# Optimization experiments

Measured on AMD Instinct MI355X. Metric: run time of the kernel, lower is better.

## Reference

```python
import jax, jax.numpy as jnp
import numpy as np

BEV_H, BEV_W, BEV_Z = 128, 128, 16
N_VOX = BEV_H * BEV_W * BEV_Z  # 262144
C = 128
N_UNMASKED = N_VOX // 4       # 65536 seed voxels (proposal > 0)
LN_EPS = 1e-5
NEG_SLOPE = 0.01


def setup_inputs() -> dict:
    key = jax.random.key(0)
    ks = jax.random.split(key, 8)
    x3d = jax.random.normal(ks[0], (1, C, N_VOX), dtype=jnp.float32)
    # disjoint unmasked/masked index sets from a permutation (proposal mask)
    perm = jax.random.permutation(ks[1], N_VOX)
    unmasked_idx = jnp.sort(perm[:N_UNMASKED]).astype(jnp.int32)
    masked_idx = jnp.sort(perm[N_UNMASKED:]).astype(jnp.int32)
    s = 0.05
    return {
        "x3d": x3d,
        "w1": jax.random.normal(ks[2], (C, C // 2), jnp.float32) * s,
        "b1": jnp.zeros((C // 2,), jnp.float32),
        "ln_g": jnp.ones((C // 2,), jnp.float32),
        "ln_b": jnp.zeros((C // 2,), jnp.float32),
        "w2": jax.random.normal(ks[3], (C // 2, C), jnp.float32) * s,
        "b2": jnp.zeros((C,), jnp.float32),
        "sdb_w": jax.random.normal(ks[4], (C, C // 2), jnp.float32) * s,
        "sdb_b": jnp.zeros((C // 2,), jnp.float32),
        "ssc_w": jax.random.normal(ks[5], (C // 2, 20), jnp.float32) * s,
        "ssc_b": jnp.zeros((20,), jnp.float32),
        "aux_w": jax.random.normal(ks[6], (C, 20), jnp.float32) * s,
        "aux_b": jnp.zeros((20,), jnp.float32),
        "unmasked_idx": unmasked_idx,
        "masked_idx": masked_idx,
    }


def _leaky(x):
    return jnp.where(x > 0, x, NEG_SLOPE * x)


def _layernorm(x, g, b):
    mu = jnp.mean(x, axis=-1, keepdims=True)
    var = jnp.mean(jnp.square(x - mu), axis=-1, keepdims=True)
    return (x - mu) * jax.lax.rsqrt(var + LN_EPS) * g + b


def reference(x3d, w1, b1, ln_g, ln_b, w2, b2, sdb_w, sdb_b, ssc_w, ssc_b,
              aux_w, aux_b, unmasked_idx, masked_idx):
    feats = x3d[0].T  # [N_vox, C]
    # gather seed (unmasked) voxel features; SGB treated as identity stand-in
    seed_feats = feats[unmasked_idx]            # [Nu, C]
    # gather masked voxel features and infill with mlp_prior:
    # Linear -> LayerNorm -> LeakyReLU -> Linear
    m = feats[masked_idx]                       # [Nm, C]
    h = _leaky(_layernorm(m @ w1 + b1, ln_g, ln_b))
    prior = h @ w2 + b2                         # [Nm, C]
    # scatter both into the dense voxel grid
    vox = jnp.zeros((N_VOX, C), x3d.dtype)
    vox = vox.at[unmasked_idx].set(seed_feats).at[masked_idx].set(prior)
    # SDB dense decode stand-in: pointwise conv C -> C/2 + LeakyReLU
    d = _leaky(vox @ sdb_w + sdb_b)             # [N_vox, C/2]
    # ssc head: per-voxel logits -> [1, 20, H, W, Z]
    ssc = d @ ssc_w + ssc_b                     # [N_vox, 20]
    ssc_logit = ssc.reshape(BEV_H, BEV_W, BEV_Z, 20).transpose(3, 0, 1, 2)[None]
    # aux sparse head on seed features
    sem_logit = seed_feats @ aux_w + aux_b      # [Nu, 20]
    return ssc_logit, sem_logit
```

## Files before the change

kernel.cpp:

```cpp
#include <hip/hip_runtime.h>
#include <hip/hip_bf16.h>


#define NVOX 262144
#define NU   65536
#define NM   196608
#define CIN  128
#define CHALF 64
#define NCLS 20
#define TR   64
#define NBLK (NVOX / TR)

#define SXS 136
#define SHS 72
#define SOS 21

#define W1F  0
#define W2F  8192
#define SDBF 16384
#define SSCF 24576
#define AUXF 26624
#define WS_WT 30720

typedef unsigned short u16;
typedef short    bf16x8 __attribute__((ext_vector_type(8)));
typedef float    f32x4  __attribute__((ext_vector_type(4)));

__device__ __forceinline__ u16 f2b(float f) {
    __hip_bfloat16 h = __float2bfloat16(f);
    return *(u16*)&h;
}

__global__ void prep_weights(const float* __restrict__ w1,  const float* __restrict__ w2,
                             const float* __restrict__ sdbw,const float* __restrict__ sscw,
                             const float* __restrict__ auxw,
                             const int* __restrict__ uidx,  const int* __restrict__ midx,
                             u16* __restrict__ ws) {
    int i = blockIdx.x * blockDim.x + threadIdx.x;
    const int stride = gridDim.x * blockDim.x;
    int* __restrict__ rank = (int*)(ws + WS_WT);
    for (int t = i; t < NU; t += stride) rank[uidx[t]] = t;
    for (int t = i; t < NM; t += stride) rank[midx[t]] = -1;
    for (; i < WS_WT; i += stride) {
        float v;
        if (i < W2F) {
            int t = i, j = t & 7, lane = (t >> 3) & 63, kc = (t >> 9) & 3, nt = t >> 11;
            int k = kc*32 + (lane >> 4)*8 + j, n = nt*16 + (lane & 15);
            v = w1[k*CHALF + n];
        } else if (i < SDBF) {
            int t = i - W2F, j = t & 7, lane = (t >> 3) & 63, kc = (t >> 9) & 1, nt = t >> 10;
            int k = kc*32 + (lane >> 4)*8 + j, n = nt*16 + (lane & 15);
            v = w2[k*CIN + n];
        } else if (i < SSCF) {
            int t = i - SDBF, j = t & 7, lane = (t >> 3) & 63, kc = (t >> 9) & 3, nt = t >> 11;
            int k = kc*32 + (lane >> 4)*8 + j, n = nt*16 + (lane & 15);
            v = sdbw[k*CHALF + n];
        } else if (i < AUXF) {
            int t = i - SSCF, j = t & 7, lane = (t >> 3) & 63, kc = (t >> 9) & 1, nt = t >> 10;
            int k = kc*32 + (lane >> 4)*8 + j, n = nt*16 + (lane & 15);
            v = (n < NCLS) ? sscw[k*NCLS + n] : 0.f;
        } else {
            int t = i - AUXF, j = t & 7, lane = (t >> 3) & 63, kc = (t >> 9) & 3, nt = t >> 11;
            int k = kc*32 + (lane >> 4)*8 + j, n = nt*16 + (lane & 15);
            v = (n < NCLS) ? auxw[k*NCLS + n] : 0.f;
        }
        ws[i] = f2b(v);
    }
}

__global__ __launch_bounds__(256, 4)
void sgn_mfma(const float* __restrict__ x3d,
              const float* __restrict__ b1,   const float* __restrict__ lng,
              const float* __restrict__ lnb,  const float* __restrict__ bb2,
              const float* __restrict__ sdbb, const float* __restrict__ sscb,
              const float* __restrict__ auxb,
              const int* __restrict__ rank,   const u16* __restrict__ wt,
              float* __restrict__ out)
{
    __shared__ __align__(16) u16 sX[TR * SXS];
    __shared__ __align__(16) u16 sH[TR * SHS];
    __shared__ __align__(16) float sOut[TR * SOS];
    __shared__ int sRank[TR];

    const int tid = threadIdx.x;
    const int p0  = (int)blockIdx.x * TR;

    const int g  = tid >> 4;
    const int v0 = (tid & 15) * 4;
    f32x4 va[4], vb[4];
    #pragma unroll
    for (int i = 0; i < 4; ++i) {
        const int c0 = i*32 + g*2;
        va[i] = *(const f32x4*)&x3d[(size_t)c0      * NVOX + p0 + v0];
        vb[i] = *(const f32x4*)&x3d[(size_t)(c0+1)  * NVOX + p0 + v0];
    }

    if (tid < TR) sRank[tid] = rank[p0 + tid];

    #pragma unroll
    for (int i = 0; i < 4; ++i) {
        const int c0 = i*32 + g*2;
        #pragma unroll
        for (int j = 0; j < 4; ++j) {
            unsigned pk = (unsigned)f2b(va[i][j]) | ((unsigned)f2b(vb[i][j]) << 16);
            *(unsigned*)&sX[(v0 + j)*SXS + c0] = pk;
        }
    }
    __syncthreads();

    const int m0   = (tid >> 6) * 16;
    const int lane = tid & 63;
    const int q    = lane >> 4;
    const int n15  = lane & 15;
    const int kq   = q * 8;


    {
        f32x4 acc[4];
        #pragma unroll
        for (int nt = 0; nt < 4; ++nt) {
            const float b = b1[nt*16 + n15];
            acc[nt] = (f32x4){b, b, b, b};
        }
        #pragma unroll
        for (int kc = 0; kc < 4; ++kc) {
            const bf16x8 a = *(const bf16x8*)&sX[(m0 + n15) * SXS + kc*32 + kq];
            #pragma unroll
            for (int nt = 0; nt < 4; ++nt) {
                const bf16x8 b = *(const bf16x8*)&wt[W1F + ((nt*4 + kc)*64 + lane)*8];
                acc[nt] = __builtin_amdgcn_mfma_f32_16x16x32_bf16(a, b, acc[nt], 0, 0, 0);
            }
        }
        float gv[4], ev[4];
        #pragma unroll
        for (int nt = 0; nt < 4; ++nt) { gv[nt] = lng[nt*16 + n15]; ev[nt] = lnb[nt*16 + n15]; }
        #pragma unroll
        for (int reg = 0; reg < 4; ++reg) {
            float s1 = acc[0][reg] + acc[1][reg] + acc[2][reg] + acc[3][reg];
            float s2 = acc[0][reg]*acc[0][reg] + acc[1][reg]*acc[1][reg]
                     + acc[2][reg]*acc[2][reg] + acc[3][reg]*acc[3][reg];
            #pragma unroll
            for (int m = 1; m <= 8; m <<= 1) {
                s1 += __shfl_xor(s1, m, 64);
                s2 += __shfl_xor(s2, m, 64);
            }
            const float mu  = s1 * (1.f/64.f);
            const float var = s2 * (1.f/64.f) - mu*mu;
            const float rs  = rsqrtf(var + 1e-5f);
            #pragma unroll
            for (int nt = 0; nt < 4; ++nt) {
                float h = (acc[nt][reg] - mu) * rs * gv[nt] + ev[nt];
                h = h > 0.f ? h : 0.01f*h;
                sH[(m0 + q*4 + reg) * SHS + nt*16 + n15] = f2b(h);
            }
        }
    }

    {
        f32x4 acc2[8];
        #pragma unroll
        for (int nt = 0; nt < 8; ++nt) {
            const float b = bb2[nt*16 + n15];
            acc2[nt] = (f32x4){b, b, b, b};
        }
        #pragma unroll
        for (int kc = 0; kc < 2; ++kc) {
            const bf16x8 a = *(const bf16x8*)&sH[(m0 + n15) * SHS + kc*32 + kq];
            #pragma unroll
            for (int nt = 0; nt < 8; ++nt) {
                const bf16x8 b = *(const bf16x8*)&wt[W2F + ((nt*2 + kc)*64 + lane)*8];
                acc2[nt] = __builtin_amdgcn_mfma_f32_16x16x32_bf16(a, b, acc2[nt], 0, 0, 0);
            }
        }
        #pragma unroll
        for (int reg = 0; reg < 4; ++reg) {
            const int row = m0 + q*4 + reg;
            if (sRank[row] < 0) {
                #pragma unroll
                for (int nt = 0; nt < 8; ++nt)
                    sX[row * SXS + nt*16 + n15] = f2b(acc2[nt][reg]);
            }
        }
    }

    {
        f32x4 accd[4];
        #pragma unroll
        for (int nt = 0; nt < 4; ++nt) {
            const float b = sdbb[nt*16 + n15];
            accd[nt] = (f32x4){b, b, b, b};
        }
        #pragma unroll
        for (int kc = 0; kc < 4; ++kc) {
            const bf16x8 a = *(const bf16x8*)&sX[(m0 + n15) * SXS + kc*32 + kq];
            #pragma unroll
            for (int nt = 0; nt < 4; ++nt) {
                const bf16x8 b = *(const bf16x8*)&wt[SDBF + ((nt*4 + kc)*64 + lane)*8];
                accd[nt] = __builtin_amdgcn_mfma_f32_16x16x32_bf16(a, b, accd[nt], 0, 0, 0);
            }
        }
        #pragma unroll
        for (int reg = 0; reg < 4; ++reg)
            #pragma unroll
            for (int nt = 0; nt < 4; ++nt) {
                float vv = accd[nt][reg];
                vv = vv > 0.f ? vv : 0.01f*vv;
                sH[(m0 + q*4 + reg) * SHS + nt*16 + n15] = f2b(vv);
            }
    }

    {
        f32x4 accs[2];
        #pragma unroll
        for (int nt = 0; nt < 2; ++nt) {
            const int col = nt*16 + n15;
            const float b = (col < NCLS) ? sscb[col] : 0.f;
            accs[nt] = (f32x4){b, b, b, b};
        }
        #pragma unroll
        for (int kc = 0; kc < 2; ++kc) {
            const bf16x8 a = *(const bf16x8*)&sH[(m0 + n15) * SHS + kc*32 + kq];
            #pragma unroll
            for (int nt = 0; nt < 2; ++nt) {
                const bf16x8 b = *(const bf16x8*)&wt[SSCF + ((nt*2 + kc)*64 + lane)*8];
                accs[nt] = __builtin_amdgcn_mfma_f32_16x16x32_bf16(a, b, accs[nt], 0, 0, 0);
            }
        }
        #pragma unroll
        for (int reg = 0; reg < 4; ++reg) {
            const int row = m0 + q*4 + reg;
            sOut[row*SOS + n15] = accs[0][reg];
            if (n15 < 4) sOut[row*SOS + 16 + n15] = accs[1][reg];
        }
    }

    f32x4 acca[2];
    {
        #pragma unroll
        for (int nt = 0; nt < 2; ++nt) {
            const int col = nt*16 + n15;
            const float b = (col < NCLS) ? auxb[col] : 0.f;
            acca[nt] = (f32x4){b, b, b, b};
        }
        #pragma unroll
        for (int kc = 0; kc < 4; ++kc) {
            const bf16x8 a = *(const bf16x8*)&sX[(m0 + n15) * SXS + kc*32 + kq];
            #pragma unroll
            for (int nt = 0; nt < 2; ++nt) {
                const bf16x8 b = *(const bf16x8*)&wt[AUXF + ((nt*4 + kc)*64 + lane)*8];
                acca[nt] = __builtin_amdgcn_mfma_f32_16x16x32_bf16(a, b, acca[nt], 0, 0, 0);
            }
        }
    }
    __syncthreads();

    #pragma unroll
    for (int jj = 0; jj < 5; ++jj) {
        const int i = tid + jj*256;
        out[(size_t)(i >> 6) * NVOX + p0 + (i & 63)] = sOut[(i & 63) * SOS + (i >> 6)];
    }

    {
        const size_t base = (size_t)NCLS * NVOX;
        #pragma unroll
        for (int reg = 0; reg < 4; ++reg) {
            const int row = m0 + q*4 + reg;
            const int rk  = sRank[row];
            if (rk >= 0) {
                out[base + (size_t)rk * NCLS + n15] = acca[0][reg];
                if (n15 < 4)
                    out[base + (size_t)rk * NCLS + 16 + n15] = acca[1][reg];
            }
        }
    }
}

extern "C" void kernel_launch(void* const* d_in, const int* in_sizes, int n_in,
                              void* d_out, int out_size, void* d_ws, size_t ws_size,
                              hipStream_t stream) {
    const float* x3d  = (const float*)d_in[0];
    const float* w1   = (const float*)d_in[1];
    const float* b1   = (const float*)d_in[2];
    const float* lng  = (const float*)d_in[3];
    const float* lnb  = (const float*)d_in[4];
    const float* w2   = (const float*)d_in[5];
    const float* bb2  = (const float*)d_in[6];
    const float* sdbw = (const float*)d_in[7];
    const float* sdbb = (const float*)d_in[8];
    const float* sscw = (const float*)d_in[9];
    const float* sscb = (const float*)d_in[10];
    const float* auxw = (const float*)d_in[11];
    const float* auxb = (const float*)d_in[12];
    const int*   uidx = (const int*)d_in[13];
    const int*   midx = (const int*)d_in[14];
    float* out = (float*)d_out;
    u16*   wt  = (u16*)d_ws;
    const int* rank = (const int*)((const char*)d_ws + WS_WT*2);

    hipLaunchKernelGGL(prep_weights, dim3(128), dim3(256), 0, stream,
                       w1, w2, sdbw, sscw, auxw, uidx, midx, wt);
    hipLaunchKernelGGL(sgn_mfma, dim3(NBLK), dim3(256), 0, stream,
                       x3d, b1, lng, lnb, bb2, sdbb, sscb, auxb,
                       rank, wt, out);
}
```

Measured before the change: 250.1 us.

## Process four tiles per block with register prefetch of next tile

Each block now loops over four 64-voxel tiles. The next tile's x3d loads and rank go into registers before the current tile's MFMA chain starts, so global load latency overlaps compute. Output stores become nontemporal, and launch bounds drop to 2 blocks per CU to make room for the prefetch registers. The cost is fewer blocks, lower occupancy and an extra barrier per tile.

```diff
diff --git a/kernel.cpp b/kernel.cpp
--- a/kernel.cpp
+++ b/kernel.cpp
@@ -9,7 +9,8 @@
 #define CHALF 64
 #define NCLS 20
 #define TR   64
-#define NBLK (NVOX / TR)
+#define TILES 4
+#define NBLK (NVOX / (TR * TILES))
 
 #define SXS 136
 #define SHS 72
@@ -68,7 +69,7 @@
     }
 }
 
-__global__ __launch_bounds__(256, 4)
+__global__ __launch_bounds__(256, 2)
 void sgn_mfma(const float* __restrict__ x3d,
               const float* __restrict__ b1,   const float* __restrict__ lng,
               const float* __restrict__ lnb,  const float* __restrict__ bb2,
@@ -82,20 +83,22 @@
     __shared__ __align__(16) float sOut[TR * SOS];
     __shared__ int sRank[TR];
 
-    const int tid = threadIdx.x;
-    const int p0  = (int)blockIdx.x * TR;
+    const int tid  = threadIdx.x;
+    const int base = (int)blockIdx.x * (TR * TILES);
 
     const int g  = tid >> 4;
     const int v0 = (tid & 15) * 4;
+
     f32x4 va[4], vb[4];
+    int rkreg = -1;
+
     #pragma unroll
     for (int i = 0; i < 4; ++i) {
         const int c0 = i*32 + g*2;
-        va[i] = *(const f32x4*)&x3d[(size_t)c0      * NVOX + p0 + v0];
-        vb[i] = *(const f32x4*)&x3d[(size_t)(c0+1)  * NVOX + p0 + v0];
+        va[i] = *(const f32x4*)&x3d[(size_t)c0      * NVOX + base + v0];
+        vb[i] = *(const f32x4*)&x3d[(size_t)(c0+1)  * NVOX + base + v0];
     }
-
-    if (tid < TR) sRank[tid] = rank[p0 + tid];
+    if (tid < TR) rkreg = rank[base + tid];
 
     #pragma unroll
     for (int i = 0; i < 4; ++i) {
@@ -106,6 +109,7 @@
             *(unsigned*)&sX[(v0 + j)*SXS + c0] = pk;
         }
     }
+    if (tid < TR) sRank[tid] = rkreg;
     __syncthreads();
 
     const int m0   = (tid >> 6) * 16;
@@ -114,164 +118,199 @@
     const int n15  = lane & 15;
     const int kq   = q * 8;
 
-
-    {
-        f32x4 acc[4];
+    #pragma unroll 1
+    for (int t = 0; t < TILES; ++t) {
+        const int p0 = base + t * TR;
+
+        if (t + 1 < TILES) {
+            #pragma unroll
+            for (int i = 0; i < 4; ++i) {
+                const int c0 = i*32 + g*2;
+                va[i] = *(const f32x4*)&x3d[(size_t)c0      * NVOX + p0 + TR + v0];
+                vb[i] = *(const f32x4*)&x3d[(size_t)(c0+1)  * NVOX + p0 + TR + v0];
+            }
+            if (tid < TR) rkreg = rank[p0 + TR + tid];
+        }
+
+        {
+            f32x4 acc[4];
+            #pragma unroll
+            for (int nt = 0; nt < 4; ++nt) {
+                const float b = b1[nt*16 + n15];
+                acc[nt] = (f32x4){b, b, b, b};
+            }
+            #pragma unroll
+            for (int kc = 0; kc < 4; ++kc) {
+                const bf16x8 a = *(const bf16x8*)&sX[(m0 + n15) * SXS + kc*32 + kq];
+                #pragma unroll
+                for (int nt = 0; nt < 4; ++nt) {
+                    const bf16x8 b = *(const bf16x8*)&wt[W1F + ((nt*4 + kc)*64 + lane)*8];
+                    acc[nt] = __builtin_amdgcn_mfma_f32_16x16x32_bf16(a, b, acc[nt], 0, 0, 0);
+                }
+            }
+            float gv[4], ev[4];
+            #pragma unroll
+            for (int nt = 0; nt < 4; ++nt) { gv[nt] = lng[nt*16 + n15]; ev[nt] = lnb[nt*16 + n15]; }
+            #pragma unroll
+            for (int reg = 0; reg < 4; ++reg) {
+                float s1 = acc[0][reg] + acc[1][reg] + acc[2][reg] + acc[3][reg];
+                float s2 = acc[0][reg]*acc[0][reg] + acc[1][reg]*acc[1][reg]
+                         + acc[2][reg]*acc[2][reg] + acc[3][reg]*acc[3][reg];
+                #pragma unroll
+                for (int m = 1; m <= 8; m <<= 1) {
+                    s1 += __shfl_xor(s1, m, 64);
+                    s2 += __shfl_xor(s2, m, 64);
+                }
+                const float mu  = s1 * (1.f/64.f);
+                const float var = s2 * (1.f/64.f) - mu*mu;
+                const float rs  = rsqrtf(var + 1e-5f);
+                #pragma unroll
+                for (int nt = 0; nt < 4; ++nt) {
+                    float h = (acc[nt][reg] - mu) * rs * gv[nt] + ev[nt];
+                    h = h > 0.f ? h : 0.01f*h;
+                    sH[(m0 + q*4 + reg) * SHS + nt*16 + n15] = f2b(h);
+                }
+            }
+        }
+
+        {
+            f32x4 acc2[8];
+            #pragma unroll
+            for (int nt = 0; nt < 8; ++nt) {
+                const float b = bb2[nt*16 + n15];
+                acc2[nt] = (f32x4){b, b, b, b};
+            }
+            #pragma unroll
+            for (int kc = 0; kc < 2; ++kc) {
+                const bf16x8 a = *(const bf16x8*)&sH[(m0 + n15) * SHS + kc*32 + kq];
+                #pragma unroll
+                for (int nt = 0; nt < 8; ++nt) {
+                    const bf16x8 b = *(const bf16x8*)&wt[W2F + ((nt*2 + kc)*64 + lane)*8];
+                    acc2[nt] = __builtin_amdgcn_mfma_f32_16x16x32_bf16(a, b, acc2[nt], 0, 0, 0);
+                }
+            }
+            #pragma unroll
+            for (int reg = 0; reg < 4; ++reg) {
+                const int row = m0 + q*4 + reg;
+                if (sRank[row] < 0) {
+                    #pragma unroll
+                    for (int nt = 0; nt < 8; ++nt)
+                        sX[row * SXS + nt*16 + n15] = f2b(acc2[nt][reg]);
+                }
+            }
+        }
+
+        {
+            f32x4 accd[4];
+            #pragma unroll
+            for (int nt = 0; nt < 4; ++nt) {
+                const float b = sdbb[nt*16 + n15];
+                accd[nt] = (f32x4){b, b, b, b};
+            }
+            #pragma unroll
+            for (int kc = 0; kc < 4; ++kc) {
+                const bf16x8 a = *(const bf16x8*)&sX[(m0 + n15) * SXS + kc*32 + kq];
+                #pragma unroll
+                for (int nt = 0; nt < 4; ++nt) {
+                    const bf16x8 b = *(const bf16x8*)&wt[SDBF + ((nt*4 + kc)*64 + lane)*8];
+                    accd[nt] = __builtin_amdgcn_mfma_f32_16x16x32_bf16(a, b, accd[nt], 0, 0, 0);
+                }
+            }
+            #pragma unroll
+            for (int reg = 0; reg < 4; ++reg)
+                #pragma unroll
+                for (int nt = 0; nt < 4; ++nt) {
+                    float vv = accd[nt][reg];
+                    vv = vv > 0.f ? vv : 0.01f*vv;
+                    sH[(m0 + q*4 + reg) * SHS + nt*16 + n15] = f2b(vv);
+                }
+        }
+
+        {
+            f32x4 accs[2];
+            #pragma unroll
+            for (int nt = 0; nt < 2; ++nt) {
+                const int col = nt*16 + n15;
+                const float b = (col < NCLS) ? sscb[col] : 0.f;
+                accs[nt] = (f32x4){b, b, b, b};
+            }
+            #pragma unroll
+            for (int kc = 0; kc < 2; ++kc) {
+                const bf16x8 a = *(const bf16x8*)&sH[(m0 + n15) * SHS + kc*32 + kq];
+                #pragma unroll
+                for (int nt = 0; nt < 2; ++nt) {
+                    const bf16x8 b = *(const bf16x8*)&wt[SSCF + ((nt*2 + kc)*64 + lane)*8];
+                    accs[nt] = __builtin_amdgcn_mfma_f32_16x16x32_bf16(a, b, accs[nt], 0, 0, 0);
+                }
+            }
+            #pragma unroll
+            for (int reg = 0; reg < 4; ++reg) {
+                const int row = m0 + q*4 + reg;
+                sOut[row*SOS + n15] = accs[0][reg];
+                if (n15 < 4) sOut[row*SOS + 16 + n15] = accs[1][reg];
+            }
+        }
+
+        f32x4 acca[2];
+        {
+            #pragma unroll
+            for (int nt = 0; nt < 2; ++nt) {
+                const int col = nt*16 + n15;
+                const float b = (col < NCLS) ? auxb[col] : 0.f;
+                acca[nt] = (f32x4){b, b, b, b};
+            }
+            #pragma unroll
+            for (int kc = 0; kc < 4; ++kc) {
+                const bf16x8 a = *(const bf16x8*)&sX[(m0 + n15) * SXS + kc*32 + kq];
+                #pragma unroll
+                for (int nt = 0; nt < 2; ++nt) {
+                    const bf16x8 b = *(const bf16x8*)&wt[AUXF + ((nt*4 + kc)*64 + lane)*8];
+                    acca[nt] = __builtin_amdgcn_mfma_f32_16x16x32_bf16(a, b, acca[nt], 0, 0, 0);
+                }
+            }
+        }
+
+        int rk4[4];
         #pragma unroll
-        for (int nt = 0; nt < 4; ++nt) {
-            const float b = b1[nt*16 + n15];
-            acc[nt] = (f32x4){b, b, b, b};
-        }
+        for (int reg = 0; reg < 4; ++reg) rk4[reg] = sRank[m0 + q*4 + reg];
+
+        __syncthreads();
+
         #pragma unroll
-        for (int kc = 0; kc < 4; ++kc) {
-            const bf16x8 a = *(const bf16x8*)&sX[(m0 + n15) * SXS + kc*32 + kq];
-            #pragma unroll
-            for (int nt = 0; nt < 4; ++nt) {
-                const bf16x8 b = *(const bf16x8*)&wt[W1F + ((nt*4 + kc)*64 + lane)*8];
-                acc[nt] = __builtin_amdgcn_mfma_f32_16x16x32_bf16(a, b, acc[nt], 0, 0, 0);
-            }
-        }
-        float gv[4], ev[4];
-        #pragma unroll
-        for (int nt = 0; nt < 4; ++nt) { gv[nt] = lng[nt*16 + n15]; ev[nt] = lnb[nt*16 + n15]; }
-        #pragma unroll
-        for (int reg = 0; reg < 4; ++reg) {
-            float s1 = acc[0][reg] + acc[1][reg] + acc[2][reg] + acc[3][reg];
-            float s2 = acc[0][reg]*acc[0][reg] + acc[1][reg]*acc[1][reg]
-                     + acc[2][reg]*acc[2][reg] + acc[3][reg]*acc[3][reg];
-            #pragma unroll
-            for (int m = 1; m <= 8; m <<= 1) {
-                s1 += __shfl_xor(s1, m, 64);
-                s2 += __shfl_xor(s2, m, 64);
-            }
-            const float mu  = s1 * (1.f/64.f);
-            const float var = s2 * (1.f/64.f) - mu*mu;
-            const float rs  = rsqrtf(var + 1e-5f);
-            #pragma unroll
-            for (int nt = 0; nt < 4; ++nt) {
-                float h = (acc[nt][reg] - mu) * rs * gv[nt] + ev[nt];
-                h = h > 0.f ? h : 0.01f*h;
-                sH[(m0 + q*4 + reg) * SHS + nt*16 + n15] = f2b(h);
-            }
-        }
-    }
-
-    {
-        f32x4 acc2[8];
-        #pragma unroll
-        for (int nt = 0; nt < 8; ++nt) {
-            const float b = bb2[nt*16 + n15];
-            acc2[nt] = (f32x4){b, b, b, b};
-        }
-        #pragma unroll
-        for (int kc = 0; kc < 2; ++kc) {
-            const bf16x8 a = *(const bf16x8*)&sH[(m0 + n15) * SHS + kc*32 + kq];
-            #pragma unroll
-            for (int nt = 0; nt < 8; ++nt) {
-                const bf16x8 b = *(const bf16x8*)&wt[W2F + ((nt*2 + kc)*64 + lane)*8];
-                acc2[nt] = __builtin_amdgcn_mfma_f32_16x16x32_bf16(a, b, acc2[nt], 0, 0, 0);
-            }
-        }
-        #pragma unroll
-        for (int reg = 0; reg < 4; ++reg) {
-            const int row = m0 + q*4 + reg;
-            if (sRank[row] < 0) {
-                #pragma unroll
-                for (int nt = 0; nt < 8; ++nt)
-                    sX[row * SXS + nt*16 + n15] = f2b(acc2[nt][reg]);
-            }
-        }
-    }
-
-    {
-        f32x4 accd[4];
-        #pragma unroll
-        for (int nt = 0; nt < 4; ++nt) {
-            const float b = sdbb[nt*16 + n15];
-            accd[nt] = (f32x4){b, b, b, b};
-        }
-        #pragma unroll
-        for (int kc = 0; kc < 4; ++kc) {
-            const bf16x8 a = *(const bf16x8*)&sX[(m0 + n15) * SXS + kc*32 + kq];
-            #pragma unroll
-            for (int nt = 0; nt < 4; ++nt) {
-                const bf16x8 b = *(const bf16x8*)&wt[SDBF + ((nt*4 + kc)*64 + lane)*8];
-                accd[nt] = __builtin_amdgcn_mfma_f32_16x16x32_bf16(a, b, accd[nt], 0, 0, 0);
-            }
-        }
-        #pragma unroll
-        for (int reg = 0; reg < 4; ++reg)
-            #pragma unroll
-            for (int nt = 0; nt < 4; ++nt) {
-                float vv = accd[nt][reg];
-                vv = vv > 0.f ? vv : 0.01f*vv;
-                sH[(m0 + q*4 + reg) * SHS + nt*16 + n15] = f2b(vv);
-            }
-    }
-
-    {
-        f32x4 accs[2];
-        #pragma unroll
-        for (int nt = 0; nt < 2; ++nt) {
-            const int col = nt*16 + n15;
-            const float b = (col < NCLS) ? sscb[col] : 0.f;
-            accs[nt] = (f32x4){b, b, b, b};
-        }
-        #pragma unroll
-        for (int kc = 0; kc < 2; ++kc) {
-            const bf16x8 a = *(const bf16x8*)&sH[(m0 + n15) * SHS + kc*32 + kq];
-            #pragma unroll
-            for (int nt = 0; nt < 2; ++nt) {
-                const bf16x8 b = *(const bf16x8*)&wt[SSCF + ((nt*2 + kc)*64 + lane)*8];
-                accs[nt] = __builtin_amdgcn_mfma_f32_16x16x32_bf16(a, b, accs[nt], 0, 0, 0);
-            }
-        }
-        #pragma unroll
-        for (int reg = 0; reg < 4; ++reg) {
-            const int row = m0 + q*4 + reg;
-            sOut[row*SOS + n15] = accs[0][reg];
-            if (n15 < 4) sOut[row*SOS + 16 + n15] = accs[1][reg];
-        }
-    }
-
-    f32x4 acca[2];
-    {
-        #pragma unroll
-        for (int nt = 0; nt < 2; ++nt) {
-            const int col = nt*16 + n15;
-            const float b = (col < NCLS) ? auxb[col] : 0.f;
-            acca[nt] = (f32x4){b, b, b, b};
-        }
-        #pragma unroll
-        for (int kc = 0; kc < 4; ++kc) {
-            const bf16x8 a = *(const bf16x8*)&sX[(m0 + n15) * SXS + kc*32 + kq];
-            #pragma unroll
-            for (int nt = 0; nt < 2; ++nt) {
-                const bf16x8 b = *(const bf16x8*)&wt[AUXF + ((nt*4 + kc)*64 + lane)*8];
-                acca[nt] = __builtin_amdgcn_mfma_f32_16x16x32_bf16(a, b, acca[nt], 0, 0, 0);
-            }
-        }
-    }
-    __syncthreads();
-
-    #pragma unroll
-    for (int jj = 0; jj < 5; ++jj) {
-        const int i = tid + jj*256;
-        out[(size_t)(i >> 6) * NVOX + p0 + (i & 63)] = sOut[(i & 63) * SOS + (i >> 6)];
-    }
-
-    {
-        const size_t base = (size_t)NCLS * NVOX;
-        #pragma unroll
-        for (int reg = 0; reg < 4; ++reg) {
-            const int row = m0 + q*4 + reg;
-            const int rk  = sRank[row];
-            if (rk >= 0) {
-                out[base + (size_t)rk * NCLS + n15] = acca[0][reg];
-                if (n15 < 4)
-                    out[base + (size_t)rk * NCLS + 16 + n15] = acca[1][reg];
-            }
-        }
+        for (int jj = 0; jj < 5; ++jj) {
+            const int i = tid + jj*256;
+            __builtin_nontemporal_store(sOut[(i & 63) * SOS + (i >> 6)],
+                &out[(size_t)(i >> 6) * NVOX + p0 + (i & 63)]);
+        }
+
+        {
+            const size_t abase = (size_t)NCLS * NVOX;
+            #pragma unroll
+            for (int reg = 0; reg < 4; ++reg) {
+                const int rk = rk4[reg];
+                if (rk >= 0) {
+                    __builtin_nontemporal_store(acca[0][reg],
+                        &out[abase + (size_t)rk * NCLS + n15]);
+                    if (n15 < 4)
+                        __builtin_nontemporal_store(acca[1][reg],
+                            &out[abase + (size_t)rk * NCLS + 16 + n15]);
+                }
+            }
+        }
+
+        if (t + 1 < TILES) {
+            #pragma unroll
+            for (int i = 0; i < 4; ++i) {
+                const int c0 = i*32 + g*2;
+                #pragma unroll
+                for (int j = 0; j < 4; ++j) {
+                    unsigned pk = (unsigned)f2b(va[i][j]) | ((unsigned)f2b(vb[i][j]) << 16);
+                    *(unsigned*)&sX[(v0 + j)*SXS + c0] = pk;
+                }
+            }
+            if (tid < TR) sRank[tid] = rkreg;
+        }
+        __syncthreads();
     }
 }
 
```

Result: slower. 397.7 us (+59.0%).

## Double rows per block so each wave reuses weight fragments across two M-tiles

Applied to the files above, without the earlier changes.

Block tile grows from 64 to 128 voxels, and each wave now computes two 16-row MFMA tiles that share every weight fragment load from global memory. This halves weight fetches per voxel and gives each wave more independent MFMAs to interleave. The load stage now converts each chunk straight into LDS instead of holding all loads in registers first, and the aux stores move before the final barrier. The cost is more registers and LDS per block, with launch bounds lowered to 2 blocks per SM, so occupancy and latency hiding may drop.

```diff
diff --git a/kernel.cpp b/kernel.cpp
--- a/kernel.cpp
+++ b/kernel.cpp
@@ -8,7 +8,7 @@
 #define CIN  128
 #define CHALF 64
 #define NCLS 20
-#define TR   64
+#define TR   128
 #define NBLK (NVOX / TR)
 
 #define SXS 136
@@ -68,7 +68,7 @@
     }
 }
 
-__global__ __launch_bounds__(256, 4)
+__global__ __launch_bounds__(256, 2)
 void sgn_mfma(const float* __restrict__ x3d,
               const float* __restrict__ b1,   const float* __restrict__ lng,
               const float* __restrict__ lnb,  const float* __restrict__ bb2,
@@ -85,193 +85,206 @@
     const int tid = threadIdx.x;
     const int p0  = (int)blockIdx.x * TR;
 
-    const int g  = tid >> 4;
-    const int v0 = (tid & 15) * 4;
-    f32x4 va[4], vb[4];
+    const int g  = tid >> 5;
+    const int v0 = (tid & 31) * 4;
     #pragma unroll
-    for (int i = 0; i < 4; ++i) {
-        const int c0 = i*32 + g*2;
-        va[i] = *(const f32x4*)&x3d[(size_t)c0      * NVOX + p0 + v0];
-        vb[i] = *(const f32x4*)&x3d[(size_t)(c0+1)  * NVOX + p0 + v0];
-    }
-
+    for (int i = 0; i < 8; ++i) {
+        const int c0 = g*2 + 16*i;
+        f32x4 va = *(const f32x4*)&x3d[(size_t)c0     * NVOX + p0 + v0];
+        f32x4 vb = *(const f32x4*)&x3d[(size_t)(c0+1) * NVOX + p0 + v0];
+        #pragma unroll
+        for (int j = 0; j < 4; ++j) {
+            unsigned pk = (unsigned)f2b(va[j]) | ((unsigned)f2b(vb[j]) << 16);
+            *(unsigned*)&sX[(v0 + j)*SXS + c0] = pk;
+        }
+    }
     if (tid < TR) sRank[tid] = rank[p0 + tid];
-
-    #pragma unroll
-    for (int i = 0; i < 4; ++i) {
-        const int c0 = i*32 + g*2;
-        #pragma unroll
-        for (int j = 0; j < 4; ++j) {
-            unsigned pk = (unsigned)f2b(va[i][j]) | ((unsigned)f2b(vb[i][j]) << 16);
-            *(unsigned*)&sX[(v0 + j)*SXS + c0] = pk;
-        }
-    }
     __syncthreads();
 
-    const int m0   = (tid >> 6) * 16;
+    const int W0   = (tid >> 6) * 32;
     const int lane = tid & 63;
     const int q    = lane >> 4;
     const int n15  = lane & 15;
     const int kq   = q * 8;
 
-
-    {
-        f32x4 acc[4];
+    {
+        f32x4 acc[2][4];
         #pragma unroll
         for (int nt = 0; nt < 4; ++nt) {
             const float b = b1[nt*16 + n15];
-            acc[nt] = (f32x4){b, b, b, b};
+            acc[0][nt] = (f32x4){b, b, b, b};
+            acc[1][nt] = (f32x4){b, b, b, b};
         }
         #pragma unroll
         for (int kc = 0; kc < 4; ++kc) {
-            const bf16x8 a = *(const bf16x8*)&sX[(m0 + n15) * SXS + kc*32 + kq];
+            const bf16x8 a0 = *(const bf16x8*)&sX[(W0      + n15) * SXS + kc*32 + kq];
+            const bf16x8 a1 = *(const bf16x8*)&sX[(W0 + 16 + n15) * SXS + kc*32 + kq];
             #pragma unroll
             for (int nt = 0; nt < 4; ++nt) {
                 const bf16x8 b = *(const bf16x8*)&wt[W1F + ((nt*4 + kc)*64 + lane)*8];
-                acc[nt] = __builtin_amdgcn_mfma_f32_16x16x32_bf16(a, b, acc[nt], 0, 0, 0);
+                acc[0][nt] = __builtin_amdgcn_mfma_f32_16x16x32_bf16(a0, b, acc[0][nt], 0, 0, 0);
+                acc[1][nt] = __builtin_amdgcn_mfma_f32_16x16x32_bf16(a1, b, acc[1][nt], 0, 0, 0);
             }
         }
         float gv[4], ev[4];
         #pragma unroll
         for (int nt = 0; nt < 4; ++nt) { gv[nt] = lng[nt*16 + n15]; ev[nt] = lnb[nt*16 + n15]; }
         #pragma unroll
-        for (int reg = 0; reg < 4; ++reg) {
-            float s1 = acc[0][reg] + acc[1][reg] + acc[2][reg] + acc[3][reg];
-            float s2 = acc[0][reg]*acc[0][reg] + acc[1][reg]*acc[1][reg]
-                     + acc[2][reg]*acc[2][reg] + acc[3][reg]*acc[3][reg];
-            #pragma unroll
-            for (int m = 1; m <= 8; m <<= 1) {
-                s1 += __shfl_xor(s1, m, 64);
-                s2 += __shfl_xor(s2, m, 64);
-            }
-            const float mu  = s1 * (1.f/64.f);
-            const float var = s2 * (1.f/64.f) - mu*mu;
-            const float rs  = rsqrtf(var + 1e-5f);
-            #pragma unroll
-            for (int nt = 0; nt < 4; ++nt) {
-                float h = (acc[nt][reg] - mu) * rs * gv[nt] + ev[nt];
-                h = h > 0.f ? h : 0.01f*h;
-                sH[(m0 + q*4 + reg) * SHS + nt*16 + n15] = f2b(h);
-            }
-        }
-    }
-
-    {
-        f32x4 acc2[8];
+        for (int mm = 0; mm < 2; ++mm)
+            #pragma unroll
+            for (int reg = 0; reg < 4; ++reg) {
+                float s1 = acc[mm][0][reg] + acc[mm][1][reg] + acc[mm][2][reg] + acc[mm][3][reg];
+                float s2 = acc[mm][0][reg]*acc[mm][0][reg] + acc[mm][1][reg]*acc[mm][1][reg]
+                         + acc[mm][2][reg]*acc[mm][2][reg] + acc[mm][3][reg]*acc[mm][3][reg];
+                #pragma unroll
+                for (int m = 1; m <= 8; m <<= 1) {
+                    s1 += __shfl_xor(s1, m, 64);
+                    s2 += __shfl_xor(s2, m, 64);
+                }
+                const float mu  = s1 * (1.f/64.f);
+                const float var = s2 * (1.f/64.f) - mu*mu;
+                const float rs  = rsqrtf(var + 1e-5f);
+                #pragma unroll
+                for (int nt = 0; nt < 4; ++nt) {
+                    float h = (acc[mm][nt][reg] - mu) * rs * gv[nt] + ev[nt];
+                    h = h > 0.f ? h : 0.01f*h;
+                    sH[(W0 + mm*16 + q*4 + reg) * SHS + nt*16 + n15] = f2b(h);
+                }
+            }
+    }
+
+    {
+        f32x4 acc2[2][8];
         #pragma unroll
         for (int nt = 0; nt < 8; ++nt) {
             const float b = bb2[nt*16 + n15];
-            acc2[nt] = (f32x4){b, b, b, b};
+            acc2[0][nt] = (f32x4){b, b, b, b};
+            acc2[1][nt] = (f32x4){b, b, b, b};
         }
         #pragma unroll
         for (int kc = 0; kc < 2; ++kc) {
-            const bf16x8 a = *(const bf16x8*)&sH[(m0 + n15) * SHS + kc*32 + kq];
+            const bf16x8 a0 = *(const bf16x8*)&sH[(W0      + n15) * SHS + kc*32 + kq];
+            const bf16x8 a1 = *(const bf16x8*)&sH[(W0 + 16 + n15) * SHS + kc*32 + kq];
             #pragma unroll
             for (int nt = 0; nt < 8; ++nt) {
                 const bf16x8 b = *(const bf16x8*)&wt[W2F + ((nt*2 + kc)*64 + lane)*8];
-                acc2[nt] = __builtin_amdgcn_mfma_f32_16x16x32_bf16(a, b, acc2[nt], 0, 0, 0);
-            }
-        }
-        #pragma unroll
-        for (int reg = 0; reg < 4; ++reg) {
-            const int row = m0 + q*4 + reg;
-            if (sRank[row] < 0) {
-                #pragma unroll
-                for (int nt = 0; nt < 8; ++nt)
-                    sX[row * SXS + nt*16 + n15] = f2b(acc2[nt][reg]);
-            }
-        }
-    }
-
-    {
-        f32x4 accd[4];
+                acc2[0][nt] = __builtin_amdgcn_mfma_f32_16x16x32_bf16(a0, b, acc2[0][nt], 0, 0, 0);
+                acc2[1][nt] = __builtin_amdgcn_mfma_f32_16x16x32_bf16(a1, b, acc2[1][nt], 0, 0, 0);
+            }
+        }
+        #pragma unroll
+        for (int mm = 0; mm < 2; ++mm)
+            #pragma unroll
+            for (int reg = 0; reg < 4; ++reg) {
+                const int row = W0 + mm*16 + q*4 + reg;
+                if (sRank[row] < 0) {
+                    #pragma unroll
+                    for (int nt = 0; nt < 8; ++nt)
+                        sX[row * SXS + nt*16 + n15] = f2b(acc2[mm][nt][reg]);
+                }
+            }
+    }
+
+    {
+        f32x4 accd[2][4];
         #pragma unroll
         for (int nt = 0; nt < 4; ++nt) {
             const float b = sdbb[nt*16 + n15];
-            accd[nt] = (f32x4){b, b, b, b};
+            accd[0][nt] = (f32x4){b, b, b, b};
+            accd[1][nt] = (f32x4){b, b, b, b};
         }
         #pragma unroll
         for (int kc = 0; kc < 4; ++kc) {
-            const bf16x8 a = *(const bf16x8*)&sX[(m0 + n15) * SXS + kc*32 + kq];
+            const bf16x8 a0 = *(const bf16x8*)&sX[(W0      + n15) * SXS + kc*32 + kq];
+            const bf16x8 a1 = *(const bf16x8*)&sX[(W0 + 16 + n15) * SXS + kc*32 + kq];
             #pragma unroll
             for (int nt = 0; nt < 4; ++nt) {
                 const bf16x8 b = *(const bf16x8*)&wt[SDBF + ((nt*4 + kc)*64 + lane)*8];
-                accd[nt] = __builtin_amdgcn_mfma_f32_16x16x32_bf16(a, b, accd[nt], 0, 0, 0);
-            }
-        }
-        #pragma unroll
-        for (int reg = 0; reg < 4; ++reg)
-            #pragma unroll
-            for (int nt = 0; nt < 4; ++nt) {
-                float vv = accd[nt][reg];
-                vv = vv > 0.f ? vv : 0.01f*vv;
-                sH[(m0 + q*4 + reg) * SHS + nt*16 + n15] = f2b(vv);
-            }
-    }
-
-    {
-        f32x4 accs[2];
+                accd[0][nt] = __builtin_amdgcn_mfma_f32_16x16x32_bf16(a0, b, accd[0][nt], 0, 0, 0);
+                accd[1][nt] = __builtin_amdgcn_mfma_f32_16x16x32_bf16(a1, b, accd[1][nt], 0, 0, 0);
+            }
+        }
+        #pragma unroll
+        for (int mm = 0; mm < 2; ++mm)
+            #pragma unroll
+            for (int reg = 0; reg < 4; ++reg)
+                #pragma unroll
+                for (int nt = 0; nt < 4; ++nt) {
+                    float vv = accd[mm][nt][reg];
+                    vv = vv > 0.f ? vv : 0.01f*vv;
+                    sH[(W0 + mm*16 + q*4 + reg) * SHS + nt*16 + n15] = f2b(vv);
+                }
+    }
+
+    {
+        f32x4 accs[2][2];
         #pragma unroll
         for (int nt = 0; nt < 2; ++nt) {
             const int col = nt*16 + n15;
             const float b = (col < NCLS) ? sscb[col] : 0.f;
-            accs[nt] = (f32x4){b, b, b, b};
+            accs[0][nt] = (f32x4){b, b, b, b};
+            accs[1][nt] = (f32x4){b, b, b, b};
         }
         #pragma unroll
         for (int kc = 0; kc < 2; ++kc) {
-            const bf16x8 a = *(const bf16x8*)&sH[(m0 + n15) * SHS + kc*32 + kq];
+            const bf16x8 a0 = *(const bf16x8*)&sH[(W0      + n15) * SHS + kc*32 + kq];
+            const bf16x8 a1 = *(const bf16x8*)&sH[(W0 + 16 + n15) * SHS + kc*32 + kq];
             #pragma unroll
             for (int nt = 0; nt < 2; ++nt) {
                 const bf16x8 b = *(const bf16x8*)&wt[SSCF + ((nt*2 + kc)*64 + lane)*8];
-                accs[nt] = __builtin_amdgcn_mfma_f32_16x16x32_bf16(a, b, accs[nt], 0, 0, 0);
-            }
-        }
-        #pragma unroll
-        for (int reg = 0; reg < 4; ++reg) {
-            const int row = m0 + q*4 + reg;
-            sOut[row*SOS + n15] = accs[0][reg];
-            if (n15 < 4) sOut[row*SOS + 16 + n15] = accs[1][reg];
-        }
-    }
-
-    f32x4 acca[2];
-    {
+                accs[0][nt] = __builtin_amdgcn_mfma_f32_16x16x32_bf16(a0, b, accs[0][nt], 0, 0, 0);
+                accs[1][nt] = __builtin_amdgcn_mfma_f32_16x16x32_bf16(a1, b, accs[1][nt], 0, 0, 0);
+            }
+        }
+        #pragma unroll
+        for (int mm = 0; mm < 2; ++mm)
+            #pragma unroll
+            for (int reg = 0; reg < 4; ++reg) {
+                const int row = W0 + mm*16 + q*4 + reg;
+                sOut[row*SOS + n15] = accs[mm][0][reg];
+                if (n15 < 4) sOut[row*SOS + 16 + n15] = accs[mm][1][reg];
+            }
+    }
+
+    {
+        f32x4 acca[2][2];
         #pragma unroll
         for (int nt = 0; nt < 2; ++nt) {
             const int col = nt*16 + n15;
             const float b = (col < NCLS) ? auxb[col] : 0.f;
-            acca[nt] = (f32x4){b, b, b, b};
+            acca[0][nt] = (f32x4){b, b, b, b};
+            acca[1][nt] = (f32x4){b, b, b, b};
         }
         #pragma unroll
         for (int kc = 0; kc < 4; ++kc) {
-            const bf16x8 a = *(const bf16x8*)&sX[(m0 + n15) * SXS + kc*32 + kq];
+            const bf16x8 a0 = *(const bf16x8*)&sX[(W0      + n15) * SXS + kc*32 + kq];
+            const bf16x8 a1 = *(const bf16x8*)&sX[(W0 + 16 + n15) * SXS + kc*32 + kq];
             #pragma unroll
             for (int nt = 0; nt < 2; ++nt) {
                 const bf16x8 b = *(const bf16x8*)&wt[AUXF + ((nt*4 + kc)*64 + lane)*8];
-                acca[nt] = __builtin_amdgcn_mfma_f32_16x16x32_bf16(a, b, acca[nt], 0, 0, 0);
-            }
-        }
+                acca[0][nt] = __builtin_amdgcn_mfma_f32_16x16x32_bf16(a0, b, acca[0][nt], 0, 0, 0);
+                acca[1][nt] = __builtin_amdgcn_mfma_f32_16x16x32_bf16(a1, b, acca[1][nt], 0, 0, 0);
+            }
+        }
+        const size_t abase = (size_t)NCLS * NVOX;
+        #pragma unroll
+        for (int mm = 0; mm < 2; ++mm)
+            #pragma unroll
+            for (int reg = 0; reg < 4; ++reg) {
+                const int rk = sRank[W0 + mm*16 + q*4 + reg];
+                if (rk >= 0) {
+                    out[abase + (size_t)rk * NCLS + n15] = acca[mm][0][reg];
+                    if (n15 < 4)
+                        out[abase + (size_t)rk * NCLS + 16 + n15] = acca[mm][1][reg];
+                }
+            }
     }
     __syncthreads();
 
     #pragma unroll
-    for (int jj = 0; jj < 5; ++jj) {
+    for (int jj = 0; jj < 10; ++jj) {
         const int i = tid + jj*256;
-        out[(size_t)(i >> 6) * NVOX + p0 + (i & 63)] = sOut[(i & 63) * SOS + (i >> 6)];
-    }
-
-    {
-        const size_t base = (size_t)NCLS * NVOX;
-        #pragma unroll
-        for (int reg = 0; reg < 4; ++reg) {
-            const int row = m0 + q*4 + reg;
-            const int rk  = sRank[row];
-            if (rk >= 0) {
-                out[base + (size_t)rk * NCLS + n15] = acca[0][reg];
-                if (n15 < 4)
-                    out[base + (size_t)rk * NCLS + 16 + n15] = acca[1][reg];
-            }
-        }
+        out[(size_t)(i >> 7) * NVOX + p0 + (i & 127)] = sOut[(i & 127) * SOS + (i >> 7)];
     }
 }
 
```

Result: slower. 261.9 us (+4.7%).

## Make blocks persistent over eight tiles with async global-to-LDS prefetch

Applied to the files above, without the earlier changes.

Each block now handles eight 64-voxel tiles in a loop instead of one. The next tile's x3d slice is prefetched directly into an LDS staging buffer with global_load_lds, and the rank values are double-buffered, so load latency overlaps with the MFMA chain of the current tile. The aux head is fused into the first GEMM's K loop, reusing the same A fragments. LDS grows by 32 KB and launch bounds drop to 2 blocks per SM, which trades occupancy for explicit overlap and leaves fewer blocks to fill the GPU.

```diff
diff --git a/kernel.cpp b/kernel.cpp
--- a/kernel.cpp
+++ b/kernel.cpp
@@ -9,7 +9,8 @@
 #define CHALF 64
 #define NCLS 20
 #define TR   64
-#define NBLK (NVOX / TR)
+#define TILES 8
+#define NBLK (NVOX / (TR * TILES))
 
 #define SXS 136
 #define SHS 72
@@ -68,7 +69,7 @@
     }
 }
 
-__global__ __launch_bounds__(256, 4)
+__global__ __launch_bounds__(256, 2)
 void sgn_mfma(const float* __restrict__ x3d,
               const float* __restrict__ b1,   const float* __restrict__ lng,
               const float* __restrict__ lnb,  const float* __restrict__ bb2,
@@ -77,201 +78,220 @@
               const int* __restrict__ rank,   const u16* __restrict__ wt,
               float* __restrict__ out)
 {
+    __shared__ __align__(16) float sStage[CIN * TR];
     __shared__ __align__(16) u16 sX[TR * SXS];
     __shared__ __align__(16) u16 sH[TR * SHS];
     __shared__ __align__(16) float sOut[TR * SOS];
-    __shared__ int sRank[TR];
-
-    const int tid = threadIdx.x;
-    const int p0  = (int)blockIdx.x * TR;
-
-    const int g  = tid >> 4;
-    const int v0 = (tid & 15) * 4;
-    f32x4 va[4], vb[4];
-    #pragma unroll
-    for (int i = 0; i < 4; ++i) {
-        const int c0 = i*32 + g*2;
-        va[i] = *(const f32x4*)&x3d[(size_t)c0      * NVOX + p0 + v0];
-        vb[i] = *(const f32x4*)&x3d[(size_t)(c0+1)  * NVOX + p0 + v0];
-    }
-
-    if (tid < TR) sRank[tid] = rank[p0 + tid];
-
-    #pragma unroll
-    for (int i = 0; i < 4; ++i) {
-        const int c0 = i*32 + g*2;
+    __shared__ int sRank[2 * TR];
+
+    const int tid  = threadIdx.x;
+    const int base = (int)blockIdx.x * (TR * TILES);
+    const int w    = tid >> 6;
+    const int l    = tid & 63;
+
+    auto STAGE = [&](int pv) {
+        const float* gs = x3d + (size_t)(w*32 + (l >> 4)) * NVOX + pv + (l & 15)*4;
+        #pragma unroll
+        for (int k = 0; k < 8; ++k)
+            __builtin_amdgcn_global_load_lds(gs + (size_t)(k*4) * NVOX,
+                                             &sStage[(w*32 + k*4) * TR],
+                                             16, 0, 0);
+    };
+
+    auto PACK = [&]() {
+        const int gch = (tid >> 4) * 8;
+        const int vp  = (tid & 15) * 4;
+        f32x4 cv[8];
+        #pragma unroll
+        for (int r = 0; r < 8; ++r)
+            cv[r] = *(const f32x4*)&sStage[(gch + r) * TR + vp];
         #pragma unroll
         for (int j = 0; j < 4; ++j) {
-            unsigned pk = (unsigned)f2b(va[i][j]) | ((unsigned)f2b(vb[i][j]) << 16);
-            *(unsigned*)&sX[(v0 + j)*SXS + c0] = pk;
-        }
-    }
+            bf16x8 row;
+            #pragma unroll
+            for (int r = 0; r < 8; ++r) ((u16*)&row)[r] = f2b(cv[r][j]);
+            *(bf16x8*)&sX[(vp + j) * SXS + gch] = row;
+        }
+    };
+
+    STAGE(base);
+    if (tid < TR) sRank[tid] = rank[base + tid];
     __syncthreads();
-
-    const int m0   = (tid >> 6) * 16;
-    const int lane = tid & 63;
+    PACK();
+    __syncthreads();
+
+    const int m0   = w * 16;
+    const int lane = l;
     const int q    = lane >> 4;
     const int n15  = lane & 15;
     const int kq   = q * 8;
 
-
-    {
-        f32x4 acc[4];
+    #pragma unroll 1
+    for (int t = 0; t < TILES; ++t) {
+        const int p0 = base + t * TR;
+        const int cb = t & 1, nb = cb ^ 1;
+        int rkn = 0;
+
+        if (t + 1 < TILES) {
+            STAGE(p0 + TR);
+            if (tid < TR) rkn = rank[p0 + TR + tid];
+        }
+
+        {
+            f32x4 acc[4], acca[2];
+            #pragma unroll
+            for (int nt = 0; nt < 4; ++nt) {
+                const float b = b1[nt*16 + n15];
+                acc[nt] = (f32x4){b, b, b, b};
+            }
+            #pragma unroll
+            for (int nt = 0; nt < 2; ++nt) {
+                const int col = nt*16 + n15;
+                const float b = (col < NCLS) ? auxb[col] : 0.f;
+                acca[nt] = (f32x4){b, b, b, b};
+            }
+            #pragma unroll
+            for (int kc = 0; kc < 4; ++kc) {
+                const bf16x8 a = *(const bf16x8*)&sX[(m0 + n15) * SXS + kc*32 + kq];
+                #pragma unroll
+                for (int nt = 0; nt < 4; ++nt) {
+                    const bf16x8 b = *(const bf16x8*)&wt[W1F + ((nt*4 + kc)*64 + lane)*8];
+                    acc[nt] = __builtin_amdgcn_mfma_f32_16x16x32_bf16(a, b, acc[nt], 0, 0, 0);
+                }
+                #pragma unroll
+                for (int nt = 0; nt < 2; ++nt) {
+                    const bf16x8 b = *(const bf16x8*)&wt[AUXF + ((nt*4 + kc)*64 + lane)*8];
+                    acca[nt] = __builtin_amdgcn_mfma_f32_16x16x32_bf16(a, b, acca[nt], 0, 0, 0);
+                }
+            }
+            {
+                const size_t abase = (size_t)NCLS * NVOX;
+                #pragma unroll
+                for (int reg = 0; reg < 4; ++reg) {
+                    const int rk = sRank[cb*TR + m0 + q*4 + reg];
+                    if (rk >= 0) {
+                        out[abase + (size_t)rk * NCLS + n15] = acca[0][reg];
+                        if (n15 < 4)
+                            out[abase + (size_t)rk * NCLS + 16 + n15] = acca[1][reg];
+                    }
+                }
+            }
+            float gv[4], ev[4];
+            #pragma unroll
+            for (int nt = 0; nt < 4; ++nt) { gv[nt] = lng[nt*16 + n15]; ev[nt] = lnb[nt*16 + n15]; }
+            #pragma unroll
+            for (int reg = 0; reg < 4; ++reg) {
+                float s1 = acc[0][reg] + acc[1][reg] + acc[2][reg] + acc[3][reg];
+                float s2 = acc[0][reg]*acc[0][reg] + acc[1][reg]*acc[1][reg]
+                         + acc[2][reg]*acc[2][reg] + acc[3][reg]*acc[3][reg];
+                #pragma unroll
+                for (int m = 1; m <= 8; m <<= 1) {
+                    s1 += __shfl_xor(s1, m, 64);
+                    s2 += __shfl_xor(s2, m, 64);
+                }
+                const float mu  = s1 * (1.f/64.f);
+                const float var = s2 * (1.f/64.f) - mu*mu;
+                const float rs  = rsqrtf(var + 1e-5f);
+                #pragma unroll
+                for (int nt = 0; nt < 4; ++nt) {
+                    float h = (acc[nt][reg] - mu) * rs * gv[nt] + ev[nt];
+                    h = h > 0.f ? h : 0.01f*h;
+                    sH[(m0 + q*4 + reg) * SHS + nt*16 + n15] = f2b(h);
+                }
+            }
+        }
+
+        {
+            f32x4 acc2[8];
+            #pragma unroll
+            for (int nt = 0; nt < 8; ++nt) {
+                const float b = bb2[nt*16 + n15];
+                acc2[nt] = (f32x4){b, b, b, b};
+            }
+            #pragma unroll
+            for (int kc = 0; kc < 2; ++kc) {
+                const bf16x8 a = *(const bf16x8*)&sH[(m0 + n15) * SHS + kc*32 + kq];
+                #pragma unroll
+                for (int nt = 0; nt < 8; ++nt) {
+                    const bf16x8 b = *(const bf16x8*)&wt[W2F + ((nt*2 + kc)*64 + lane)*8];
+                    acc2[nt] = __builtin_amdgcn_mfma_f32_16x16x32_bf16(a, b, acc2[nt], 0, 0, 0);
+                }
+            }
+            #pragma unroll
+            for (int reg = 0; reg < 4; ++reg) {
+                const int row = m0 + q*4 + reg;
+                if (sRank[cb*TR + row] < 0) {
+                    #pragma unroll
+                    for (int nt = 0; nt < 8; ++nt)
+                        sX[row * SXS + nt*16 + n15] = f2b(acc2[nt][reg]);
+                }
+            }
+        }
+
+        {
+            f32x4 accd[4];
+            #pragma unroll
+            for (int nt = 0; nt < 4; ++nt) {
+                const float b = sdbb[nt*16 + n15];
+                accd[nt] = (f32x4){b, b, b, b};
+            }
+            #pragma unroll
+            for (int kc = 0; kc < 4; ++kc) {
+                const bf16x8 a = *(const bf16x8*)&sX[(m0 + n15) * SXS + kc*32 + kq];
+                #pragma unroll
+                for (int nt = 0; nt < 4; ++nt) {
+                    const bf16x8 b = *(const bf16x8*)&wt[SDBF + ((nt*4 + kc)*64 + lane)*8];
+                    accd[nt] = __builtin_amdgcn_mfma_f32_16x16x32_bf16(a, b, accd[nt], 0, 0, 0);
+                }
+            }
+            #pragma unroll
+            for (int reg = 0; reg < 4; ++reg)
+                #pragma unroll
+                for (int nt = 0; nt < 4; ++nt) {
+                    float vv = accd[nt][reg];
+                    vv = vv > 0.f ? vv : 0.01f*vv;
+                    sH[(m0 + q*4 + reg) * SHS + nt*16 + n15] = f2b(vv);
+                }
+        }
+
+        {
+            f32x4 accs[2];
+            #pragma unroll
+            for (int nt = 0; nt < 2; ++nt) {
+                const int col = nt*16 + n15;
+                const float b = (col < NCLS) ? sscb[col] : 0.f;
+                accs[nt] = (f32x4){b, b, b, b};
+            }
+            #pragma unroll
+            for (int kc = 0; kc < 2; ++kc) {
+                const bf16x8 a = *(const bf16x8*)&sH[(m0 + n15) * SHS + kc*32 + kq];
+                #pragma unroll
+                for (int nt = 0; nt < 2; ++nt) {
+                    const bf16x8 b = *(const bf16x8*)&wt[SSCF + ((nt*2 + kc)*64 + lane)*8];
+                    accs[nt] = __builtin_amdgcn_mfma_f32_16x16x32_bf16(a, b, accs[nt], 0, 0, 0);
+                }
+            }
+            #pragma unroll
+            for (int reg = 0; reg < 4; ++reg) {
+                const int row = m0 + q*4 + reg;
+                sOut[row*SOS + n15] = accs[0][reg];
+                if (n15 < 4) sOut[row*SOS + 16 + n15] = accs[1][reg];
+            }
+        }
+
+        __syncthreads();
+
         #pragma unroll
-        for (int nt = 0; nt < 4; ++nt) {
-            const float b = b1[nt*16 + n15];
-            acc[nt] = (f32x4){b, b, b, b};
-        }
-        #pragma unroll
-        for (int kc = 0; kc < 4; ++kc) {
-            const bf16x8 a = *(const bf16x8*)&sX[(m0 + n15) * SXS + kc*32 + kq];
-            #pragma unroll
-            for (int nt = 0; nt < 4; ++nt) {
-                const bf16x8 b = *(const bf16x8*)&wt[W1F + ((nt*4 + kc)*64 + lane)*8];
-                acc[nt] = __builtin_amdgcn_mfma_f32_16x16x32_bf16(a, b, acc[nt], 0, 0, 0);
-            }
-        }
-        float gv[4], ev[4];
-        #pragma unroll
-        for (int nt = 0; nt < 4; ++nt) { gv[nt] = lng[nt*16 + n15]; ev[nt] = lnb[nt*16 + n15]; }
-        #pragma unroll
-        for (int reg = 0; reg < 4; ++reg) {
-            float s1 = acc[0][reg] + acc[1][reg] + acc[2][reg] + acc[3][reg];
-            float s2 = acc[0][reg]*acc[0][reg] + acc[1][reg]*acc[1][reg]
-                     + acc[2][reg]*acc[2][reg] + acc[3][reg]*acc[3][reg];
-            #pragma unroll
-            for (int m = 1; m <= 8; m <<= 1) {
-                s1 += __shfl_xor(s1, m, 64);
-                s2 += __shfl_xor(s2, m, 64);
-            }
-            const float mu  = s1 * (1.f/64.f);
-            const float var = s2 * (1.f/64.f) - mu*mu;
-            const float rs  = rsqrtf(var + 1e-5f);
-            #pragma unroll
-            for (int nt = 0; nt < 4; ++nt) {
-                float h = (acc[nt][reg] - mu) * rs * gv[nt] + ev[nt];
-                h = h > 0.f ? h : 0.01f*h;
-                sH[(m0 + q*4 + reg) * SHS + nt*16 + n15] = f2b(h);
-            }
-        }
-    }
-
-    {
-        f32x4 acc2[8];
-        #pragma unroll
-        for (int nt = 0; nt < 8; ++nt) {
-            const float b = bb2[nt*16 + n15];
-            acc2[nt] = (f32x4){b, b, b, b};
-        }
-        #pragma unroll
-        for (int kc = 0; kc < 2; ++kc) {
-            const bf16x8 a = *(const bf16x8*)&sH[(m0 + n15) * SHS + kc*32 + kq];
-            #pragma unroll
-            for (int nt = 0; nt < 8; ++nt) {
-                const bf16x8 b = *(const bf16x8*)&wt[W2F + ((nt*2 + kc)*64 + lane)*8];
-                acc2[nt] = __builtin_amdgcn_mfma_f32_16x16x32_bf16(a, b, acc2[nt], 0, 0, 0);
-            }
-        }
-        #pragma unroll
-        for (int reg = 0; reg < 4; ++reg) {
-            const int row = m0 + q*4 + reg;
-            if (sRank[row] < 0) {
-                #pragma unroll
-                for (int nt = 0; nt < 8; ++nt)
-                    sX[row * SXS + nt*16 + n15] = f2b(acc2[nt][reg]);
-            }
-        }
-    }
-
-    {
-        f32x4 accd[4];
-        #pragma unroll
-        for (int nt = 0; nt < 4; ++nt) {
-            const float b = sdbb[nt*16 + n15];
-            accd[nt] = (f32x4){b, b, b, b};
-        }
-        #pragma unroll
-        for (int kc = 0; kc < 4; ++kc) {
-            const bf16x8 a = *(const bf16x8*)&sX[(m0 + n15) * SXS + kc*32 + kq];
-            #pragma unroll
-            for (int nt = 0; nt < 4; ++nt) {
-                const bf16x8 b = *(const bf16x8*)&wt[SDBF + ((nt*4 + kc)*64 + lane)*8];
-                accd[nt] = __builtin_amdgcn_mfma_f32_16x16x32_bf16(a, b, accd[nt], 0, 0, 0);
-            }
-        }
-        #pragma unroll
-        for (int reg = 0; reg < 4; ++reg)
-            #pragma unroll
-            for (int nt = 0; nt < 4; ++nt) {
-                float vv = accd[nt][reg];
-                vv = vv > 0.f ? vv : 0.01f*vv;
-                sH[(m0 + q*4 + reg) * SHS + nt*16 + n15] = f2b(vv);
-            }
-    }
-
-    {
-        f32x4 accs[2];
-        #pragma unroll
-        for (int nt = 0; nt < 2; ++nt) {
-            const int col = nt*16 + n15;
-            const float b = (col < NCLS) ? sscb[col] : 0.f;
-            accs[nt] = (f32x4){b, b, b, b};
-        }
-        #pragma unroll
-        for (int kc = 0; kc < 2; ++kc) {
-            const bf16x8 a = *(const bf16x8*)&sH[(m0 + n15) * SHS + kc*32 + kq];
-            #pragma unroll
-            for (int nt = 0; nt < 2; ++nt) {
-                const bf16x8 b = *(const bf16x8*)&wt[SSCF + ((nt*2 + kc)*64 + lane)*8];
-                accs[nt] = __builtin_amdgcn_mfma_f32_16x16x32_bf16(a, b, accs[nt], 0, 0, 0);
-            }
-        }
-        #pragma unroll
-        for (int reg = 0; reg < 4; ++reg) {
-            const int row = m0 + q*4 + reg;
-            sOut[row*SOS + n15] = accs[0][reg];
-            if (n15 < 4) sOut[row*SOS + 16 + n15] = accs[1][reg];
-        }
-    }
-
-    f32x4 acca[2];
-    {
-        #pragma unroll
-        for (int nt = 0; nt < 2; ++nt) {
-            const int col = nt*16 + n15;
-            const float b = (col < NCLS) ? auxb[col] : 0.f;
-            acca[nt] = (f32x4){b, b, b, b};
-        }
-        #pragma unroll
-        for (int kc = 0; kc < 4; ++kc) {
-            const bf16x8 a = *(const bf16x8*)&sX[(m0 + n15) * SXS + kc*32 + kq];
-            #pragma unroll
-            for (int nt = 0; nt < 2; ++nt) {
-                const bf16x8 b = *(const bf16x8*)&wt[AUXF + ((nt*4 + kc)*64 + lane)*8];
-                acca[nt] = __builtin_amdgcn_mfma_f32_16x16x32_bf16(a, b, acca[nt], 0, 0, 0);
-            }
-        }
-    }
-    __syncthreads();
-
-    #pragma unroll
-    for (int jj = 0; jj < 5; ++jj) {
-        const int i = tid + jj*256;
-        out[(size_t)(i >> 6) * NVOX + p0 + (i & 63)] = sOut[(i & 63) * SOS + (i >> 6)];
-    }
-
-    {
-        const size_t base = (size_t)NCLS * NVOX;
-        #pragma unroll
-        for (int reg = 0; reg < 4; ++reg) {
-            const int row = m0 + q*4 + reg;
-            const int rk  = sRank[row];
-            if (rk >= 0) {
-                out[base + (size_t)rk * NCLS + n15] = acca[0][reg];
-                if (n15 < 4)
-                    out[base + (size_t)rk * NCLS + 16 + n15] = acca[1][reg];
-            }
-        }
+        for (int jj = 0; jj < 5; ++jj) {
+            const int i = tid + jj*256;
+            out[(size_t)(i >> 6) * NVOX + p0 + (i & 63)] = sOut[(i & 63) * SOS + (i >> 6)];
+        }
+
+        if (t + 1 < TILES) {
+            PACK();
+            if (tid < TR) sRank[nb*TR + tid] = rkn;
+        }
+        __syncthreads();
     }
 }
 
```

After: 361.1 us. 1.44x slower.
